# Kernel optimization log

Hardware: AMD Instinct MI355X
Metric: run time of the kernel (lower is better)

## Reference

```python
import jax, jax.numpy as jnp
import numpy as np

N_LAYERS = 24  # number of recurrent applications of the shared HashLinear


def setup_inputs() -> dict:
    key = jax.random.key(0)
    ks = jax.random.split(key, 9)
    B, D_IN, N, N_OUT = 1024, 784, 4096, 10
    s_in = 1.0 / np.sqrt(D_IN)
    s_h = 1.0 / np.sqrt(N)
    x = jax.random.normal(ks[0], (B, D_IN), jnp.float32)
    # nn.Linear(prod(input_dim), 2*n_units)
    W_in = jax.random.uniform(ks[1], (2 * N, D_IN), jnp.float32, -s_in, s_in)
    b_in = jax.random.uniform(ks[2], (2 * N,), jnp.float32, -s_in, s_in)
    # HashLinear(n_units, n_units, period=1, 'hash'): learnable +/-1 context key + shared linear
    key_sp = jnp.where(jax.random.bernoulli(ks[3], 0.5, (1, N)), 1.0, -1.0).astype(jnp.float32)
    W_sp = jax.random.uniform(ks[4], (N, N), jnp.float32, -s_h, s_h)
    b_sp = jax.random.uniform(ks[5], (N,), jnp.float32, -s_h, s_h)
    # HashLinear(n_units, 10, period=1, 'hash')
    key_f = jnp.where(jax.random.bernoulli(ks[6], 0.5, (1, N)), 1.0, -1.0).astype(jnp.float32)
    W_f = jax.random.uniform(ks[7], (N_OUT, N), jnp.float32, -s_h, s_h)
    b_f = jax.random.uniform(ks[8], (N_OUT,), jnp.float32, -s_h, s_h)
    return {"x": x, "W_in": W_in, "b_in": b_in, "key_sp": key_sp, "W_sp": W_sp,
            "b_sp": b_sp, "key_f": key_f, "W_f": W_f, "b_f": b_f, "time": 0}


def _hash_linear(xa, xb, o, W, b):
    # Superposition HashLinear: same shared weight applied to both streams,
    # each modulated by the +/-1 context key o ([n_in]).
    ya = (xa * o) @ W.T + b
    yb = (xb * o) @ W.T + b
    return ya, yb


def reference(x, W_in, b_in, key_sp, W_sp, b_sp, key_f, W_f, b_f, time):
    N = W_sp.shape[0]
    r = x @ W_in.T + b_in                 # [B, 2N]
    r_a, r_b = r[:, :N], r[:, N:]         # torch.split(r, n_units, 1)
    pre0 = r_a
    r_a, r_b = jax.nn.relu(r_a), jax.nn.relu(r_b)
    o = key_sp[time % key_sp.shape[0]]    # period=1, time=0 in the module

    def step(carry, _):
        a, b2 = carry
        ya, yb = _hash_linear(a, b2, o, W_sp, b_sp)
        return (jax.nn.relu(ya), jax.nn.relu(yb)), ya  # collect preactivation r_a

    (r_a, r_b), pres = jax.lax.scan(step, (r_a, r_b), None, length=N_LAYERS)
    of = key_f[time % key_f.shape[0]]
    out_a, out_b = _hash_linear(r_a, r_b, of, W_f, b_f)  # [B,10], [B,10]
    preactivations = jnp.concatenate([pre0[None], pres], axis=0)  # [N_LAYERS+1, B, N]
    return (out_a, out_b, preactivations)
```

## Files before the change

### kernel.cpp

```cpp
#include <hip/hip_runtime.h>
#include <hip/hip_bf16.h>
#include <stdint.h>

typedef __bf16 bf16x8 __attribute__((ext_vector_type(8)));
typedef float  f32x4  __attribute__((ext_vector_type(4)));

#define NH      4096
#define MB      1024
#define M2      2048
#define DIN     784
#define KPAD    832
#define N_IN    8192
#define NLAYERS 24
#define NOUT    10

#define ASL     (128 * 64)
#define SLOT    (2 * ASL)

__device__ __forceinline__ unsigned short f2bf(float x) {
  union { float f; unsigned u; } v; v.f = x;
  unsigned r = v.u + 0x7FFFu + ((v.u >> 16) & 1u);
  return (unsigned short)(r >> 16);
}
__device__ __forceinline__ float bf2f(unsigned short u) {
  union { unsigned u; float f; } v; v.u = ((unsigned)u) << 16; return v.f;
}

__device__ __forceinline__ void async16(const void* g, void* l) {
  __builtin_amdgcn_global_load_lds(
      (const __attribute__((address_space(1))) void*)g,
      (__attribute__((address_space(3))) void*)l, 16, 0, 0);
}

__global__ void k_conv_wsp(const float* __restrict__ W, const float* __restrict__ o,
                           unsigned short* __restrict__ out) {
  size_t i = ((size_t)blockIdx.x * blockDim.x + threadIdx.x) * 4;
  if (i >= (size_t)NH * NH) return;
  float4 w = *reinterpret_cast<const float4*>(W + i);
  int k = (int)(i & (NH - 1));
  float4 ov = *reinterpret_cast<const float4*>(o + k);
  ushort4 r;
  r.x = f2bf(w.x * ov.x); r.y = f2bf(w.y * ov.y);
  r.z = f2bf(w.z * ov.z); r.w = f2bf(w.w * ov.w);
  *reinterpret_cast<ushort4*>(out + i) = r;
}

__global__ void k_conv_pad(const float* __restrict__ in, unsigned short* __restrict__ out,
                           int rows, int kin, int kout) {
  size_t i = (size_t)blockIdx.x * blockDim.x + threadIdx.x;
  if (i >= (size_t)rows * kout) return;
  int r = (int)(i / kout), c = (int)(i % kout);
  out[i] = (c < kin) ? f2bf(in[(size_t)r * kin + c]) : (unsigned short)0;
}

__device__ __forceinline__ void gemm_core(
    const unsigned short* __restrict__ Ag, const unsigned short* __restrict__ Bg,
    int K, int bm, int bn, unsigned short* lds, f32x4 acc[4][4])
{
  const int t    = threadIdx.x;
  const int lane = t & 63;
  const int wave = t >> 6;
  const int wm   = wave >> 1;
  const int wn   = wave & 1;
  const int l15  = lane & 15;
  const int lkb  = (lane >> 4) * 16;

  const int srow = t >> 3;
  const int sb   = ((t & 7) * 16) ^ ((srow & 7) << 4);
  const unsigned aG0 = (unsigned)((bm + srow) * K + (sb >> 1));
  const unsigned bG0 = (unsigned)((bn + srow) * K + (sb >> 1));

  auto STAGE = [&](int bufIdx, int k0) {
    unsigned short* s = lds + bufIdx * SLOT;
#pragma unroll
    for (int j = 0; j < 4; ++j)
      async16(Ag + aG0 + (unsigned)(j * 32 * K + k0), s + t * 8 + j * 2048);
#pragma unroll
    for (int j = 0; j < 4; ++j)
      async16(Bg + bG0 + (unsigned)(j * 32 * K + k0), s + ASL + t * 8 + j * 2048);
  };

  int aRd[2][4], bRd[2][4];
#pragma unroll
  for (int kk = 0; kk < 2; ++kk)
#pragma unroll
    for (int i = 0; i < 4; ++i) {
      const int ra = wm * 64 + i * 16 + l15;
      aRd[kk][i] = (ra * 128 + ((kk * 64 + lkb) ^ ((ra & 7) << 4))) >> 1;
      const int rb = wn * 64 + i * 16 + l15;
      bRd[kk][i] = (rb * 128 + ((kk * 64 + lkb) ^ ((rb & 7) << 4))) >> 1;
    }

  const int nt = K >> 6;
  STAGE(0, 0);
  asm volatile("s_waitcnt vmcnt(0)" ::: "memory");
  __builtin_amdgcn_s_barrier();

  int buf = 0;
  for (int kt = 0; kt < nt; ++kt) {
    if (kt + 1 < nt) STAGE(buf ^ 1, (kt + 1) << 6);
    const unsigned short* base = lds + buf * SLOT;
    __builtin_amdgcn_s_setprio(1);
#pragma unroll
    for (int kk = 0; kk < 2; ++kk) {
      bf16x8 a[4], b[4];
#pragma unroll
      for (int i = 0; i < 4; ++i) a[i] = *reinterpret_cast<const bf16x8*>(base + aRd[kk][i]);
#pragma unroll
      for (int i = 0; i < 4; ++i) b[i] = *reinterpret_cast<const bf16x8*>(base + ASL + bRd[kk][i]);
#pragma unroll
      for (int mi = 0; mi < 4; ++mi)
#pragma unroll
        for (int ni = 0; ni < 4; ++ni)
          acc[mi][ni] = __builtin_amdgcn_mfma_f32_16x16x32_bf16(a[mi], b[ni], acc[mi][ni], 0, 0, 0);
    }
    __builtin_amdgcn_s_setprio(0);
    if (kt + 1 < nt) {
      asm volatile("s_waitcnt vmcnt(0)" ::: "memory");
      __builtin_amdgcn_s_barrier();
    }
    buf ^= 1;
  }
}

__global__ __launch_bounds__(256, 2) void k_gemm_layer(
    const unsigned short* __restrict__ A, const unsigned short* __restrict__ W,
    const float* __restrict__ bias, float* __restrict__ preact,
    unsigned short* __restrict__ Anext)
{
  __shared__ __align__(16) unsigned short lds[2 * SLOT];
  const int bid = blockIdx.x;
  const int xcd = bid & 7;
  const int idx = bid >> 3;
  const int bm  = (idx >> 2) * 128;
  const int bn  = (xcd * 4 + (idx & 3)) * 128;
  f32x4 acc[4][4] = {};
  gemm_core(A, W, NH, bm, bn, lds, acc);

  const int lane = threadIdx.x & 63;
  const int wave = threadIdx.x >> 6;
  const int wm = (wave >> 1) * 64, wn = (wave & 1) * 64;
  const int l15 = lane & 15;
#pragma unroll
  for (int mi = 0; mi < 4; ++mi) {
    const int gm0 = bm + wm + mi * 16 + (lane >> 4) * 4;
#pragma unroll
    for (int ni = 0; ni < 4; ++ni) {
      const int gn = bn + wn + ni * 16 + l15;
      const float bv = bias[gn];
#pragma unroll
      for (int r = 0; r < 4; ++r) {
        const int gm = gm0 + r;
        const float y = acc[mi][ni][r] + bv;
        if (gm < MB) preact[(size_t)gm * NH + gn] = y;
        Anext[(size_t)gm * NH + gn] = f2bf(y > 0.f ? y : 0.f);
      }
    }
  }
}

__global__ __launch_bounds__(256, 2) void k_gemm_in(
    const unsigned short* __restrict__ X, const unsigned short* __restrict__ W,
    const float* __restrict__ bias, float* __restrict__ preact0,
    unsigned short* __restrict__ A0)
{
  __shared__ __align__(16) unsigned short lds[2 * SLOT];
  const int bid = blockIdx.x;
  const int xcd = bid & 7;
  const int idx = bid >> 3;
  const int bm  = (idx >> 3) * 128;
  const int bn  = (xcd * 8 + (idx & 7)) * 128;
  f32x4 acc[4][4] = {};
  gemm_core(X, W, KPAD, bm, bn, lds, acc);

  const int lane = threadIdx.x & 63;
  const int wave = threadIdx.x >> 6;
  const int wm = (wave >> 1) * 64, wn = (wave & 1) * 64;
  const int l15 = lane & 15;
#pragma unroll
  for (int mi = 0; mi < 4; ++mi) {
    const int gm0 = bm + wm + mi * 16 + (lane >> 4) * 4;
#pragma unroll
    for (int ni = 0; ni < 4; ++ni) {
      const int gn = bn + wn + ni * 16 + l15;
      const float bv = bias[gn];
#pragma unroll
      for (int r = 0; r < 4; ++r) {
        const int gm = gm0 + r;
        const float y = acc[mi][ni][r] + bv;
        const unsigned short rl = f2bf(y > 0.f ? y : 0.f);
        if (gn < NH) {
          preact0[(size_t)gm * NH + gn] = y;
          A0[(size_t)gm * NH + gn] = rl;
        } else {
          A0[(size_t)(MB + gm) * NH + (gn - NH)] = rl;
        }
      }
    }
  }
}

__global__ void k_final(const unsigned short* __restrict__ A,
                        const float* __restrict__ Wf, const float* __restrict__ of,
                        const float* __restrict__ bf_, float* __restrict__ out)
{
  const int m = blockIdx.x;
  const int t = threadIdx.x;
  float accj[NOUT] = {};
  for (int k = t; k < NH; k += 256) {
    const float a = bf2f(A[(size_t)m * NH + k]) * of[k];
#pragma unroll
    for (int j = 0; j < NOUT; ++j) accj[j] += a * Wf[j * NH + k];
  }
  __shared__ float red[4][NOUT];
#pragma unroll
  for (int j = 0; j < NOUT; ++j) {
    float v = accj[j];
    for (int off = 32; off > 0; off >>= 1) v += __shfl_down(v, off);
    if ((t & 63) == 0) red[t >> 6][j] = v;
  }
  __syncthreads();
  if (t < NOUT) {
    const float s = red[0][t] + red[1][t] + red[2][t] + red[3][t] + bf_[t];
    out[(size_t)m * NOUT + t] = s;
  }
}

extern "C" void kernel_launch(void* const* d_in, const int* in_sizes, int n_in,
                              void* d_out, int out_size, void* d_ws, size_t ws_size,
                              hipStream_t stream) {
  const float* x     = (const float*)d_in[0];
  const float* W_in  = (const float*)d_in[1];
  const float* b_in  = (const float*)d_in[2];
  const float* keysp = (const float*)d_in[3];
  const float* W_sp  = (const float*)d_in[4];
  const float* b_sp  = (const float*)d_in[5];
  const float* keyf  = (const float*)d_in[6];
  const float* W_f   = (const float*)d_in[7];
  const float* b_f   = (const float*)d_in[8];

  float* out    = (float*)d_out;
  float* preact = out + (size_t)2 * MB * NOUT;

  char* ws = (char*)d_ws;
  unsigned short* Wsp_bf = (unsigned short*)ws;  ws += (size_t)NH * NH * 2;
  unsigned short* A0     = (unsigned short*)ws;  ws += (size_t)M2 * NH * 2;
  unsigned short* A1     = (unsigned short*)ws;  ws += (size_t)M2 * NH * 2;
  unsigned short* Win_bf = (unsigned short*)ws;  ws += (size_t)N_IN * KPAD * 2;
  unsigned short* X_bf   = (unsigned short*)ws;  ws += (size_t)MB * KPAD * 2;

  k_conv_wsp<<<(NH * (size_t)NH / 4 + 255) / 256, 256, 0, stream>>>(W_sp, keysp, Wsp_bf);
  k_conv_pad<<<((size_t)N_IN * KPAD + 255) / 256, 256, 0, stream>>>(W_in, Win_bf, N_IN, DIN, KPAD);
  k_conv_pad<<<((size_t)MB * KPAD + 255) / 256, 256, 0, stream>>>(x, X_bf, MB, DIN, KPAD);

  k_gemm_in<<<512, 256, 0, stream>>>(X_bf, Win_bf, b_in, preact, A0);

  unsigned short* Ain = A0;
  unsigned short* Aout = A1;
  for (int tlay = 0; tlay < NLAYERS; ++tlay) {
    float* pre = preact + (size_t)(tlay + 1) * MB * NH;
    k_gemm_layer<<<512, 256, 0, stream>>>(Ain, Wsp_bf, b_sp, pre, Aout);
    unsigned short* tmp = Ain; Ain = Aout; Aout = tmp;
  }

  k_final<<<M2, 256, 0, stream>>>(Ain, W_f, keyf, b_f, out);
}
```

Baseline: 1.610 ms.

## Fuse input, recurrent layers and final projection into one persistent kernel

Replaces the input GEMM launch, the 24 per-layer GEMM launches and the final projection launch with a single persistent kernel of 512 blocks. Blocks are ordered by per-row-band atomic counters: a block starts layer L once the 32 tiles of its row band from layer L-1 have posted. This removes per-launch gaps and the full-grid barrier between layers, so adjacent layers can overlap across bands. In exchange it depends on all 512 blocks being co-resident to avoid deadlock, and it adds spin-wait and memset overhead.

```diff
diff --git a/kernel.cpp b/kernel.cpp
--- a/kernel.cpp
+++ b/kernel.cpp
@@ -123,106 +123,122 @@
   }
 }
 
-__global__ __launch_bounds__(256, 2) void k_gemm_layer(
-    const unsigned short* __restrict__ A, const unsigned short* __restrict__ W,
-    const float* __restrict__ bias, float* __restrict__ preact,
-    unsigned short* __restrict__ Anext)
+__global__ __launch_bounds__(256, 2) void k_net(
+    const unsigned short* __restrict__ X, const unsigned short* __restrict__ Win,
+    const float* __restrict__ b_in,
+    const unsigned short* __restrict__ Wsp, const float* __restrict__ b_sp,
+    unsigned short* __restrict__ A0, unsigned short* __restrict__ A1,
+    float* __restrict__ preact, float* __restrict__ out,
+    const float* __restrict__ Wf, const float* __restrict__ of_,
+    const float* __restrict__ bf_, int* __restrict__ flags)
 {
   __shared__ __align__(16) unsigned short lds[2 * SLOT];
-  const int bid = blockIdx.x;
-  const int xcd = bid & 7;
-  const int idx = bid >> 3;
-  const int bm  = (idx >> 2) * 128;
-  const int bn  = (xcd * 4 + (idx & 3)) * 128;
-  f32x4 acc[4][4] = {};
-  gemm_core(A, W, NH, bm, bn, lds, acc);
-
-  const int lane = threadIdx.x & 63;
-  const int wave = threadIdx.x >> 6;
-  const int wm = (wave >> 1) * 64, wn = (wave & 1) * 64;
-  const int l15 = lane & 15;
-#pragma unroll
-  for (int mi = 0; mi < 4; ++mi) {
-    const int gm0 = bm + wm + mi * 16 + (lane >> 4) * 4;
-#pragma unroll
-    for (int ni = 0; ni < 4; ++ni) {
-      const int gn = bn + wn + ni * 16 + l15;
-      const float bv = bias[gn];
-#pragma unroll
-      for (int r = 0; r < 4; ++r) {
-        const int gm = gm0 + r;
-        const float y = acc[mi][ni][r] + bv;
-        if (gm < MB) preact[(size_t)gm * NH + gn] = y;
-        Anext[(size_t)gm * NH + gn] = f2bf(y > 0.f ? y : 0.f);
-      }
-    }
-  }
-}
-
-__global__ __launch_bounds__(256, 2) void k_gemm_in(
-    const unsigned short* __restrict__ X, const unsigned short* __restrict__ W,
-    const float* __restrict__ bias, float* __restrict__ preact0,
-    unsigned short* __restrict__ A0)
-{
-  __shared__ __align__(16) unsigned short lds[2 * SLOT];
-  const int bid = blockIdx.x;
-  const int xcd = bid & 7;
-  const int idx = bid >> 3;
-  const int bm  = (idx >> 3) * 128;
-  const int bn  = (xcd * 8 + (idx & 7)) * 128;
-  f32x4 acc[4][4] = {};
-  gemm_core(X, W, KPAD, bm, bn, lds, acc);
-
-  const int lane = threadIdx.x & 63;
-  const int wave = threadIdx.x >> 6;
-  const int wm = (wave >> 1) * 64, wn = (wave & 1) * 64;
-  const int l15 = lane & 15;
-#pragma unroll
-  for (int mi = 0; mi < 4; ++mi) {
-    const int gm0 = bm + wm + mi * 16 + (lane >> 4) * 4;
-#pragma unroll
-    for (int ni = 0; ni < 4; ++ni) {
-      const int gn = bn + wn + ni * 16 + l15;
-      const float bv = bias[gn];
-#pragma unroll
-      for (int r = 0; r < 4; ++r) {
-        const int gm = gm0 + r;
-        const float y = acc[mi][ni][r] + bv;
-        const unsigned short rl = f2bf(y > 0.f ? y : 0.f);
-        if (gn < NH) {
-          preact0[(size_t)gm * NH + gn] = y;
-          A0[(size_t)gm * NH + gn] = rl;
-        } else {
-          A0[(size_t)(MB + gm) * NH + (gn - NH)] = rl;
+  __shared__ float red[4][NOUT];
+  const int bid  = blockIdx.x;
+  const int xcd  = bid & 7;
+  const int idx  = bid >> 3;
+  const int t    = threadIdx.x;
+  const int lane = t & 63;
+  const int wave = t >> 6;
+  const int wm   = (wave >> 1) * 64, wn = (wave & 1) * 64;
+  const int l15  = lane & 15;
+
+  auto post = [&](int L, int band) {
+    asm volatile("s_waitcnt vmcnt(0)" ::: "memory");
+    __syncthreads();
+    if (t == 0)
+      __hip_atomic_fetch_add(&flags[L * 16 + band], 1,
+                             __ATOMIC_RELEASE, __HIP_MEMORY_SCOPE_AGENT);
+  };
+  auto waitband = [&](int L, int band) {
+    if (t == 0) {
+      while (__hip_atomic_load(&flags[L * 16 + band],
+                               __ATOMIC_ACQUIRE, __HIP_MEMORY_SCOPE_AGENT) < 32)
+        __builtin_amdgcn_s_sleep(2);
+    }
+    __syncthreads();
+  };
+
+  {
+    const int bm = (idx >> 3) * 128;
+    const int bn = (xcd * 8 + (idx & 7)) * 128;
+    f32x4 acc[4][4] = {};
+    gemm_core(X, Win, KPAD, bm, bn, lds, acc);
+#pragma unroll
+    for (int mi = 0; mi < 4; ++mi) {
+      const int gm0 = bm + wm + mi * 16 + (lane >> 4) * 4;
+#pragma unroll
+      for (int ni = 0; ni < 4; ++ni) {
+        const int gn = bn + wn + ni * 16 + l15;
+        const float bv = b_in[gn];
+#pragma unroll
+        for (int r = 0; r < 4; ++r) {
+          const int gm = gm0 + r;
+          const float y = acc[mi][ni][r] + bv;
+          const unsigned short rl = f2bf(y > 0.f ? y : 0.f);
+          if (gn < NH) {
+            preact[(size_t)gm * NH + gn] = y;
+            A0[(size_t)gm * NH + gn] = rl;
+          } else {
+            A0[(size_t)(MB + gm) * NH + (gn - NH)] = rl;
+          }
         }
       }
     }
-  }
-}
-
-__global__ void k_final(const unsigned short* __restrict__ A,
-                        const float* __restrict__ Wf, const float* __restrict__ of,
-                        const float* __restrict__ bf_, float* __restrict__ out)
-{
-  const int m = blockIdx.x;
-  const int t = threadIdx.x;
-  float accj[NOUT] = {};
-  for (int k = t; k < NH; k += 256) {
-    const float a = bf2f(A[(size_t)m * NH + k]) * of[k];
-#pragma unroll
-    for (int j = 0; j < NOUT; ++j) accj[j] += a * Wf[j * NH + k];
-  }
-  __shared__ float red[4][NOUT];
-#pragma unroll
-  for (int j = 0; j < NOUT; ++j) {
-    float v = accj[j];
-    for (int off = 32; off > 0; off >>= 1) v += __shfl_down(v, off);
-    if ((t & 63) == 0) red[t >> 6][j] = v;
-  }
-  __syncthreads();
-  if (t < NOUT) {
-    const float s = red[0][t] + red[1][t] + red[2][t] + red[3][t] + bf_[t];
-    out[(size_t)m * NOUT + t] = s;
+    post(0, (bn >= NH ? 8 : 0) + (bm >> 7));
+  }
+
+  const int bm   = (idx >> 2) * 128;
+  const int bn   = (xcd * 4 + (idx & 3)) * 128;
+  const int band = bm >> 7;
+  for (int lay = 0; lay < NLAYERS; ++lay) {
+    const unsigned short* Ain = (lay & 1) ? A1 : A0;
+    unsigned short*      Aout = (lay & 1) ? A0 : A1;
+    waitband(lay, band);
+    f32x4 acc[4][4] = {};
+    gemm_core(Ain, Wsp, NH, bm, bn, lds, acc);
+    float* pre = preact + (size_t)(lay + 1) * MB * NH;
+#pragma unroll
+    for (int mi = 0; mi < 4; ++mi) {
+      const int gm0 = bm + wm + mi * 16 + (lane >> 4) * 4;
+#pragma unroll
+      for (int ni = 0; ni < 4; ++ni) {
+        const int gn = bn + wn + ni * 16 + l15;
+        const float bv = b_sp[gn];
+#pragma unroll
+        for (int r = 0; r < 4; ++r) {
+          const int gm = gm0 + r;
+          const float y = acc[mi][ni][r] + bv;
+          if (gm < MB) pre[(size_t)gm * NH + gn] = y;
+          Aout[(size_t)gm * NH + gn] = f2bf(y > 0.f ? y : 0.f);
+        }
+      }
+    }
+    post(lay + 1, band);
+  }
+
+  waitband(NLAYERS, bid >> 5);
+  const unsigned short* Afin = A0;
+  for (int rr = 0; rr < 4; ++rr) {
+    const int m = bid * 4 + rr;
+    float accj[NOUT];
+#pragma unroll
+    for (int j = 0; j < NOUT; ++j) accj[j] = 0.f;
+    for (int k = t; k < NH; k += 256) {
+      const float a = bf2f(Afin[(size_t)m * NH + k]) * of_[k];
+#pragma unroll
+      for (int j = 0; j < NOUT; ++j) accj[j] += a * Wf[j * NH + k];
+    }
+#pragma unroll
+    for (int j = 0; j < NOUT; ++j) {
+      float v = accj[j];
+      for (int off = 32; off > 0; off >>= 1) v += __shfl_down(v, off);
+      if ((t & 63) == 0) red[t >> 6][j] = v;
+    }
+    __syncthreads();
+    if (t < NOUT)
+      out[(size_t)m * NOUT + t] = red[0][t] + red[1][t] + red[2][t] + red[3][t] + bf_[t];
+    __syncthreads();
   }
 }
 
@@ -248,20 +264,14 @@
   unsigned short* A1     = (unsigned short*)ws;  ws += (size_t)M2 * NH * 2;
   unsigned short* Win_bf = (unsigned short*)ws;  ws += (size_t)N_IN * KPAD * 2;
   unsigned short* X_bf   = (unsigned short*)ws;  ws += (size_t)MB * KPAD * 2;
+  int* flags             = (int*)ws;             ws += (NLAYERS + 1) * 16 * sizeof(int);
+
+  hipMemsetAsync(flags, 0, (NLAYERS + 1) * 16 * sizeof(int), stream);
 
   k_conv_wsp<<<(NH * (size_t)NH / 4 + 255) / 256, 256, 0, stream>>>(W_sp, keysp, Wsp_bf);
   k_conv_pad<<<((size_t)N_IN * KPAD + 255) / 256, 256, 0, stream>>>(W_in, Win_bf, N_IN, DIN, KPAD);
   k_conv_pad<<<((size_t)MB * KPAD + 255) / 256, 256, 0, stream>>>(x, X_bf, MB, DIN, KPAD);
 
-  k_gemm_in<<<512, 256, 0, stream>>>(X_bf, Win_bf, b_in, preact, A0);
-
-  unsigned short* Ain = A0;
-  unsigned short* Aout = A1;
-  for (int tlay = 0; tlay < NLAYERS; ++tlay) {
-    float* pre = preact + (size_t)(tlay + 1) * MB * NH;
-    k_gemm_layer<<<512, 256, 0, stream>>>(Ain, Wsp_bf, b_sp, pre, Aout);
-    unsigned short* tmp = Ain; Ain = Aout; Aout = tmp;
-  }
-
-  k_final<<<M2, 256, 0, stream>>>(Ain, W_f, keyf, b_f, out);
-}
+  k_net<<<512, 256, 0, stream>>>(X_bf, Win_bf, b_in, Wsp_bf, b_sp,
+                                 A0, A1, preact, out, W_f, keyf, b_f, flags);
+}
```

Measured after the change: 2.848 ms. 76.9% more time.
